# Kernel tuning notes

Hardware: AMD Instinct MI355X
Metric: run time of the kernel (lower is better)

The kernel has to match this reference:

```python
import jax, jax.numpy as jnp
import numpy as np

DIM = 768
N_HEADS = 12
HEAD_DIM = DIM // N_HEADS
B, S = 2, 4096


def setup_inputs() -> dict:
    key = jax.random.key(0)
    k_x, k_wqkv, k_bqkv, k_wout, k_bout = jax.random.split(key, 5)
    scale_in = 1.0 / np.sqrt(DIM)
    return {
        "x": jax.random.normal(k_x, (B, S, DIM), dtype=jnp.float32),
        "Wqkv": jax.random.normal(k_wqkv, (DIM, 3 * DIM), dtype=jnp.float32) * scale_in,
        "bqkv": jax.random.normal(k_bqkv, (3 * DIM,), dtype=jnp.float32) * 0.02,
        "Wout": jax.random.normal(k_wout, (DIM, DIM), dtype=jnp.float32) * scale_in,
        "bout": jax.random.normal(k_bout, (DIM,), dtype=jnp.float32) * 0.02,
    }


def reference(x, Wqkv, bqkv, Wout, bout):
    b, s, d = x.shape
    qkv = (x @ Wqkv + bqkv).reshape(b, s, 3, N_HEADS, HEAD_DIM)
    qkv = jnp.transpose(qkv, (2, 0, 3, 1, 4))  # [3, B, H, S, hd]
    q, k, v = qkv[0], qkv[1], qkv[2]
    scale = HEAD_DIM ** -0.5
    attn = jnp.einsum('bhqd,bhkd->bhqk', q, k) * scale  # [B, H, S, S]
    causal_mask = jnp.triu(jnp.ones((s, s), dtype=bool), k=1)
    attn = jnp.where(causal_mask[None, None], -jnp.inf, attn)
    attn = jax.nn.softmax(attn, axis=-1)
    out = jnp.einsum('bhqk,bhkd->bhqd', attn, v)  # [B, H, S, hd]
    out = jnp.transpose(out, (0, 2, 1, 3)).reshape(b, s, d)
    return out @ Wout + bout
```

## Files before the change

### kernel.cpp

```cpp
#include <hip/hip_runtime.h>
#include <hip/hip_bf16.h>
#include <math.h>

#define DIM 768
#define NH 12
#define HD 64
#define BATCH 2
#define SEQ 4096
#define MTOT (BATCH * SEQ)

#define QSCALE 0.1803368801111244f

typedef unsigned short u16;
typedef __bf16 bf16x8 __attribute__((ext_vector_type(8)));
typedef float  f32x4  __attribute__((ext_vector_type(4)));
typedef float  f32x16 __attribute__((ext_vector_type(16)));
typedef unsigned short u16x4 __attribute__((ext_vector_type(4)));
typedef unsigned short u16x8 __attribute__((ext_vector_type(8)));
typedef unsigned u32x4 __attribute__((ext_vector_type(4)));

__device__ inline u16 f2bf(float f) {
    unsigned u = __builtin_bit_cast(unsigned, f);
    u += 0x7fffu + ((u >> 16) & 1u);
    return (u16)(u >> 16);
}

#if defined(__has_builtin) && __has_builtin(__builtin_amdgcn_cvt_pk_bf16_f32)
#define HAVE_PK_BF16 1
__device__ inline unsigned pk2bf(float a, float b) {
    auto v = __builtin_amdgcn_cvt_pk_bf16_f32(a, b);
    return __builtin_bit_cast(unsigned, v);
}
#else
#define HAVE_PK_BF16 0
__device__ inline unsigned pk2bf(float a, float b) {
    return (unsigned)f2bf(a) | ((unsigned)f2bf(b) << 16);
}
#endif

__device__ inline f32x16 mfma32(bf16x8 a, bf16x8 b, f32x16 c) {
    return __builtin_amdgcn_mfma_f32_32x32x16_bf16(a, b, c, 0, 0, 0);
}

__device__ inline void gl2lds16(const u16* g, u16* l) {
    __builtin_amdgcn_global_load_lds(
        (const __attribute__((address_space(1))) void*)g,
        (__attribute__((address_space(3))) void*)l,
        16, 0, 0);
}

__global__ __launch_bounds__(256)
void prep_fused(const float* __restrict__ x, u16* __restrict__ Xb,
                const float* __restrict__ Wqkv, u16* __restrict__ Wqt,
                const float* __restrict__ Wout, u16* __restrict__ Wot)
{
    const int bid = blockIdx.x;
    if (bid < 3072) {
        const int i = bid * 256 + threadIdx.x;
        float4 a = ((const float4*)x)[i * 2];
        float4 b = ((const float4*)x)[i * 2 + 1];
        u16x8 o;
        o[0] = f2bf(a.x); o[1] = f2bf(a.y); o[2] = f2bf(a.z); o[3] = f2bf(a.w);
        o[4] = f2bf(b.x); o[5] = f2bf(b.y); o[6] = f2bf(b.z); o[7] = f2bf(b.w);
        ((u16x8*)Xb)[i] = o;
        return;
    }
    __shared__ float tile[32][33];
    const float* src; u16* dst; int R, C, bx, by;
    if (bid < 3072 + 1728) {
        const int t2 = bid - 3072;
        src = Wqkv; dst = Wqt; R = 768; C = 2304;
        bx = t2 % 72; by = t2 / 72;
    } else {
        const int t2 = bid - 4800;
        src = Wout; dst = Wot; R = 768; C = 768;
        bx = t2 % 24; by = t2 / 24;
    }
    const int c0 = bx * 32, r0 = by * 32;
    const int tx = threadIdx.x & 31, ty = threadIdx.x >> 5;
#pragma unroll
    for (int i = 0; i < 4; ++i) {
        int row = ty * 4 + i;
        tile[row][tx] = src[(size_t)(r0 + row) * C + c0 + tx];
    }
    __syncthreads();
#pragma unroll
    for (int i = 0; i < 4; ++i) {
        int crow = ty * 4 + i;
        dst[(size_t)(c0 + crow) * R + r0 + tx] = f2bf(tile[tx][crow]);
    }
}

__device__ inline void gemm_lds_mainloop(const u16* __restrict__ Ag,
                                         const u16* __restrict__ Bg,
                                         int m0, int n0, int w, int lane,
                                         u16 (*As)[64 * 64], u16 (*Bs)[64 * 64],
                                         f32x16 acc[2][2])
{
    const int lc32 = lane & 31, hi = lane >> 5;
    const int wm = (w & 1) * 64, wn = (w >> 1) * 64;
    const int drow = lane >> 3;
    const int dp   = lane & 7;

#pragma unroll
    for (int mi = 0; mi < 2; ++mi)
#pragma unroll
        for (int nj = 0; nj < 2; ++nj)
            acc[mi][nj] = f32x16{};

    int trA[2], kcA[2], lr0[2];
#pragma unroll
    for (int i = 0; i < 2; ++i) {
        const int r = w * 16 + i * 8 + drow;
        const int g = dp ^ (r & 7);
        trA[i] = 2 * r + (g >> 2);
        kcA[i] = g & 3;
        lr0[i] = (w * 16 + i * 8) * 64;
    }

#pragma unroll
    for (int i = 0; i < 2; ++i) {
        gl2lds16(Ag + (size_t)(m0 + trA[i]) * 768 + kcA[i] * 8, &As[0][lr0[i]]);
        gl2lds16(Bg + (size_t)(n0 + trA[i]) * 768 + kcA[i] * 8, &Bs[0][lr0[i]]);
    }
#pragma unroll
    for (int i = 0; i < 2; ++i) {
        gl2lds16(Ag + (size_t)(m0 + trA[i]) * 768 + 32 + kcA[i] * 8, &As[1][lr0[i]]);
        gl2lds16(Bg + (size_t)(n0 + trA[i]) * 768 + 32 + kcA[i] * 8, &Bs[1][lr0[i]]);
    }

    int cur = 0;
    for (int ks = 0; ks < 24; ++ks) {
        if (ks + 1 < 24) { asm volatile("s_waitcnt vmcnt(4)" ::: "memory"); }
        else             { asm volatile("s_waitcnt vmcnt(0)" ::: "memory"); }
        __builtin_amdgcn_s_barrier();

        if (ks + 2 < 24) {
            const int nb = (cur >= 1) ? (cur - 1) : 2;
            const int k0 = (ks + 2) * 32;
#pragma unroll
            for (int i = 0; i < 2; ++i) {
                gl2lds16(Ag + (size_t)(m0 + trA[i]) * 768 + k0 + kcA[i] * 8,
                         &As[nb][lr0[i]]);
                gl2lds16(Bg + (size_t)(n0 + trA[i]) * 768 + k0 + kcA[i] * 8,
                         &Bs[nb][lr0[i]]);
            }
        }

        bf16x8 af[2][2], bfr[2][2];
#pragma unroll
        for (int mi = 0; mi < 2; ++mi)
#pragma unroll
            for (int kh = 0; kh < 2; ++kh) {
                const int m = wm + mi * 32 + lc32;
                const int r = m >> 1;
                const int p = ((m & 1) * 4 + kh * 2 + hi) ^ (r & 7);
                af[mi][kh] = *(const bf16x8*)&As[cur][r * 64 + p * 8];
            }
#pragma unroll
        for (int nj = 0; nj < 2; ++nj)
#pragma unroll
            for (int kh = 0; kh < 2; ++kh) {
                const int n = wn + nj * 32 + lc32;
                const int r = n >> 1;
                const int p = ((n & 1) * 4 + kh * 2 + hi) ^ (r & 7);
                bfr[nj][kh] = *(const bf16x8*)&Bs[cur][r * 64 + p * 8];
            }

        __builtin_amdgcn_s_setprio(1);
#pragma unroll
        for (int mi = 0; mi < 2; ++mi)
#pragma unroll
            for (int nj = 0; nj < 2; ++nj) {
                acc[mi][nj] = mfma32(af[mi][0], bfr[nj][0], acc[mi][nj]);
                acc[mi][nj] = mfma32(af[mi][1], bfr[nj][1], acc[mi][nj]);
            }
        __builtin_amdgcn_s_setprio(0);

        cur = (cur == 2) ? 0 : cur + 1;
    }
}

__global__ __launch_bounds__(256, 3)
void gemm_qkv_mfma(const u16* __restrict__ A, const u16* __restrict__ Bt,
                   const float* __restrict__ bias,
                   u16* __restrict__ Qb, u16* __restrict__ Kb, u16* __restrict__ Vt)
{
    __shared__ u16 As[3][64 * 64];
    __shared__ u16 Bs[3][64 * 64];
    const int bid = blockIdx.x;
    const int swz = (bid & 7) * 144 + (bid >> 3);
    const int m0 = (swz / 18) * 128;
    const int n0 = (swz % 18) * 128;
    const int t = threadIdx.x;
    const int w = t >> 6, lane = t & 63;
    const int lc32 = lane & 31, hi = lane >> 5;
    const int wm = (w & 1) * 64, wn = (w >> 1) * 64;

    f32x16 acc[2][2];
    gemm_lds_mainloop(A, Bt, m0, n0, w, lane, As, Bs, acc);

    __syncthreads();

    const int b  = m0 >> 12;
    const int s0 = (m0 & 4095) + wm;
    const int nbase = n0 + wn;
    const int three = nbase / 768;
    const int rem   = nbase - three * 768;
    const int h     = rem >> 6;
    const int bh    = b * NH + h;

    if (three < 2) {
        u16* dst = (three == 0) ? Qb : Kb;
        const float qs = (three == 0) ? QSCALE : 1.0f;
#pragma unroll
        for (int nj = 0; nj < 2; ++nj) {
            const int d = nj * 32 + lc32;
            const float bi = bias[nbase + d];
#pragma unroll
            for (int mi = 0; mi < 2; ++mi)
#pragma unroll
                for (int r = 0; r < 16; ++r) {
                    const int s = s0 + mi * 32 + (r & 3) + 8 * (r >> 2) + 4 * hi;
                    dst[((size_t)bh * SEQ + s) * HD + d] = f2bf((acc[mi][nj][r] + bi) * qs);
                }
        }
    } else {
        u16* scr = (w < 2) ? (&As[0][0] + w * 4352)
                           : (&Bs[0][0] + (w - 2) * 4352);
#pragma unroll
        for (int nj = 0; nj < 2; ++nj) {
            const int d = nj * 32 + lc32;
            const float bi = bias[nbase + d];
#pragma unroll
            for (int mi = 0; mi < 2; ++mi)
#pragma unroll
                for (int r = 0; r < 16; ++r) {
                    const int s = mi * 32 + (r & 3) + 8 * (r >> 2) + 4 * hi;
                    scr[d * 68 + s] = f2bf(acc[mi][nj][r] + bi);
                }
        }
        const size_t vbase = (size_t)bh * HD * SEQ + s0;
#pragma unroll
        for (int p = 0; p < 16; ++p) {
            const int d = p * 4 + (lane >> 4);
            const int s = (lane & 15) * 4;
            u16x4 v4 = *(const u16x4*)&scr[d * 68 + s];
            *(u16x4*)&Vt[vbase + (size_t)d * SEQ + s] = v4;
        }
    }
}

__global__ __launch_bounds__(256, 3)
void gemm_out_mfma(const u16* __restrict__ A, const u16* __restrict__ Bt,
                   const float* __restrict__ bias, float* __restrict__ C)
{
    __shared__ u16 As[3][64 * 64];
    __shared__ u16 Bs[3][32 * 64];
    const int bid = blockIdx.x;
    const int swz = (bid & 7) * 96 + (bid >> 3);
    const int m0 = (swz / 12) * 128;
    const int n0 = (swz % 12) * 64;
    const int t = threadIdx.x;
    const int w = t >> 6, lane = t & 63;
    const int lc32 = lane & 31, hi = lane >> 5;
    const int wm = (w & 1) * 64, wn = (w >> 1) * 32;
    const int drow = lane >> 3;
    const int dp   = lane & 7;

    f32x16 acc[2];
    acc[0] = f32x16{};
    acc[1] = f32x16{};

    int trA[2], kcA[2], lr0[2];
#pragma unroll
    for (int i = 0; i < 2; ++i) {
        const int r = w * 16 + i * 8 + drow;
        const int g = dp ^ (r & 7);
        trA[i] = 2 * r + (g >> 2);
        kcA[i] = g & 3;
        lr0[i] = (w * 16 + i * 8) * 64;
    }
    const int gB  = dp ^ drow;
    const int trB = 2 * (w * 8 + drow) + (gB >> 2);
    const int kcB = gB & 3;
    const int lrB = (w * 8) * 64;

#pragma unroll
    for (int i = 0; i < 2; ++i)
        gl2lds16(A + (size_t)(m0 + trA[i]) * 768 + kcA[i] * 8, &As[0][lr0[i]]);
    gl2lds16(Bt + (size_t)(n0 + trB) * 768 + kcB * 8, &Bs[0][lrB]);
#pragma unroll
    for (int i = 0; i < 2; ++i)
        gl2lds16(A + (size_t)(m0 + trA[i]) * 768 + 32 + kcA[i] * 8, &As[1][lr0[i]]);
    gl2lds16(Bt + (size_t)(n0 + trB) * 768 + 32 + kcB * 8, &Bs[1][lrB]);

    int cur = 0;
    for (int ks = 0; ks < 24; ++ks) {
        if (ks + 1 < 24) { asm volatile("s_waitcnt vmcnt(3)" ::: "memory"); }
        else             { asm volatile("s_waitcnt vmcnt(0)" ::: "memory"); }
        __builtin_amdgcn_s_barrier();

        if (ks + 2 < 24) {
            const int nb = (cur >= 1) ? (cur - 1) : 2;
            const int k0 = (ks + 2) * 32;
#pragma unroll
            for (int i = 0; i < 2; ++i)
                gl2lds16(A + (size_t)(m0 + trA[i]) * 768 + k0 + kcA[i] * 8,
                         &As[nb][lr0[i]]);
            gl2lds16(Bt + (size_t)(n0 + trB) * 768 + k0 + kcB * 8, &Bs[nb][lrB]);
        }

        bf16x8 af[2][2], bfr[2];
#pragma unroll
        for (int mi = 0; mi < 2; ++mi)
#pragma unroll
            for (int kh = 0; kh < 2; ++kh) {
                const int m = wm + mi * 32 + lc32;
                const int r = m >> 1;
                const int p = ((m & 1) * 4 + kh * 2 + hi) ^ (r & 7);
                af[mi][kh] = *(const bf16x8*)&As[cur][r * 64 + p * 8];
            }
#pragma unroll
        for (int kh = 0; kh < 2; ++kh) {
            const int n = wn + lc32;
            const int r = n >> 1;
            const int p = ((n & 1) * 4 + kh * 2 + hi) ^ (r & 7);
            bfr[kh] = *(const bf16x8*)&Bs[cur][r * 64 + p * 8];
        }

        __builtin_amdgcn_s_setprio(1);
#pragma unroll
        for (int mi = 0; mi < 2; ++mi) {
            acc[mi] = mfma32(af[mi][0], bfr[0], acc[mi]);
            acc[mi] = mfma32(af[mi][1], bfr[1], acc[mi]);
        }
        __builtin_amdgcn_s_setprio(0);

        cur = (cur == 2) ? 0 : cur + 1;
    }

    const int col = n0 + wn + lc32;
    const float bi = bias[col];
#pragma unroll
    for (int mi = 0; mi < 2; ++mi)
#pragma unroll
        for (int r = 0; r < 16; ++r) {
            const int row = m0 + wm + mi * 32 + (r & 3) + 8 * (r >> 2) + 4 * hi;
            C[(size_t)row * 768 + col] = acc[mi][r] + bi;
        }
}

__global__ __launch_bounds__(256, 4)
void flash_attn(const u16* __restrict__ Qg, const u16* __restrict__ Kg,
                const u16* __restrict__ Vtg, u16* __restrict__ Og)
{
    const int bh   = blockIdx.x;
    const int qt   = 63 - (int)blockIdx.y;
    const int b    = bh / NH, h = bh % NH;
    const int t    = threadIdx.x;
    const int w    = t >> 6;
    const int wq   = w >> 1;
    const int wk   = w & 1;
    const int lane = t & 63;
    const int lc32 = lane & 31;
    const int hi   = lane >> 5;
    const int drow = lane >> 3;
    const int dp   = lane & 7;

    __shared__ u16 Ks[2][64 * 64];
    __shared__ u16 Vs[2][64 * 64];

    const u16* Qp = Qg  + (size_t)bh * SEQ * HD;
    const u16* Kp = Kg  + (size_t)bh * SEQ * HD;
    const u16* Vp = Vtg + (size_t)bh * HD * SEQ;
    float* Vscr = (float*)&Vs[0][0];
    float* Lx   = (float*)&Ks[0][0];

    const int qrow0 = qt * 64 + wq * 32;

    bf16x8 qa[4];
#pragma unroll
    for (int ds = 0; ds < 4; ++ds)
        qa[ds] = *(const bf16x8*)
            &Qp[(size_t)(qrow0 + lc32) * HD + ds * 16 + hi * 8];

    f32x16 o2[2];
    o2[0] = f32x16{};
    o2[1] = f32x16{};
    float l_r = 0.f;

#pragma unroll
    for (int i = 0; i < 2; ++i) {
        const int r0  = w * 16 + i * 8;
        const int row = r0 + drow;
        const int gc  = dp ^ (row & 7);
        gl2lds16(Kp + (size_t)row * HD + gc * 8, &Ks[0][r0 * 64]);
        gl2lds16(Vp + (size_t)row * SEQ + gc * 8, &Vs[0][r0 * 64]);
    }
    __syncthreads();

    for (int tk = 0; tk <= qt; ++tk) {
        const int kb  = tk * 64;
        const int cur = tk & 1;

        if (tk < qt) {
            const int kbn = kb + 64;
#pragma unroll
            for (int i = 0; i < 2; ++i) {
                const int r0  = w * 16 + i * 8;
                const int row = r0 + drow;
                const int gc  = dp ^ (row & 7);
                gl2lds16(Kp + (size_t)(kbn + row) * HD + gc * 8,
                         &Ks[1 - cur][r0 * 64]);
                gl2lds16(Vp + (size_t)row * SEQ + kbn + gc * 8,
                         &Vs[1 - cur][r0 * 64]);
            }
        }

        f32x16 sacc = {};
        {
            const int row = wk * 32 + lc32;
            const int sw  = row & 7;
            __builtin_amdgcn_s_setprio(1);
#pragma unroll
            for (int ds = 0; ds < 4; ++ds) {
                bf16x8 kf = *(const bf16x8*)
                    &Ks[cur][row * 64 + (((ds * 2 + hi) ^ sw) * 8)];
                sacc = mfma32(kf, qa[ds], sacc);
            }
            __builtin_amdgcn_s_setprio(0);
        }

        if (tk == qt) {
            const int q = qrow0 + lc32;
#pragma unroll
            for (int r = 0; r < 16; ++r) {
                const int key = kb + wk * 32 + (r & 3) + 8 * (r >> 2) + 4 * hi;
                if (key > q) sacc[r] = -1e30f;
            }
        }

        float pv[16];
#pragma unroll
        for (int r = 0; r < 16; ++r)
            pv[r] = __builtin_amdgcn_exp2f(sacc[r]);

        l_r += (((pv[0] + pv[1]) + (pv[2] + pv[3]))
              + ((pv[4] + pv[5]) + (pv[6] + pv[7])))
             + (((pv[8] + pv[9]) + (pv[10] + pv[11]))
              + ((pv[12] + pv[13]) + (pv[14] + pv[15])));

        bf16x8 pa[2];
#pragma unroll
        for (int s = 0; s < 2; ++s) {
            unsigned w0 = pk2bf(pv[8 * s + 0], pv[8 * s + 1]);
            unsigned w1 = pk2bf(pv[8 * s + 2], pv[8 * s + 3]);
            unsigned w2 = pk2bf(pv[8 * s + 4], pv[8 * s + 5]);
            unsigned w3 = pk2bf(pv[8 * s + 6], pv[8 * s + 7]);
            asm("v_permlane32_swap_b32 %0, %1" : "+v"(w0), "+v"(w2));
            asm("v_permlane32_swap_b32 %0, %1" : "+v"(w1), "+v"(w3));
            u32x4 tw;
            tw[0] = w0; tw[1] = w1; tw[2] = w2; tw[3] = w3;
            pa[s] = __builtin_bit_cast(bf16x8, tw);
        }

        __builtin_amdgcn_s_setprio(1);
#pragma unroll
        for (int dt = 0; dt < 2; ++dt) {
            const int row = dt * 32 + lc32;
            const int sw  = row & 7;
#pragma unroll
            for (int s = 0; s < 2; ++s) {
                bf16x8 vf = *(const bf16x8*)
                    &Vs[cur][row * 64 + (((wk * 4 + s * 2 + hi) ^ sw) * 8)];
                o2[dt] = mfma32(pa[s], vf, o2[dt]);
            }
        }
        __builtin_amdgcn_s_setprio(0);

        __syncthreads();
    }

    const float lt = l_r + __shfl_xor(l_r, 32);

    if (wk == 1) {
#pragma unroll
        for (int dt = 0; dt < 2; ++dt)
#pragma unroll
            for (int r = 0; r < 16; ++r) {
                const int ql = (r & 3) + 8 * (r >> 2) + 4 * hi;
                Vscr[wq * 2048 + ql * 64 + dt * 32 + lc32] = o2[dt][r];
            }
        if (lane < 32) Lx[wq * 32 + lc32] = lt;
    }
    __syncthreads();
    if (wk == 0) {
        const float linv_q = 1.0f / (lt + Lx[wq * 32 + lc32]);
#pragma unroll
        for (int r = 0; r < 16; ++r) {
            const int ql   = (r & 3) + 8 * (r >> 2) + 4 * hi;
            const float li = __shfl(linv_q, ql);
            const int q = qrow0 + ql;
            const size_t base = ((size_t)(b * SEQ + q)) * DIM + h * HD + lc32;
#pragma unroll
            for (int dt = 0; dt < 2; ++dt) {
                const float ov = o2[dt][r]
                    + Vscr[wq * 2048 + ql * 64 + dt * 32 + lc32];
                Og[base + dt * 32] = f2bf(ov * li);
            }
        }
    }
}

extern "C" void kernel_launch(void* const* d_in, const int* in_sizes, int n_in,
                              void* d_out, int out_size, void* d_ws, size_t ws_size,
                              hipStream_t stream)
{
    const float* x    = (const float*)d_in[0];
    const float* Wqkv = (const float*)d_in[1];
    const float* bqkv = (const float*)d_in[2];
    const float* Wout = (const float*)d_in[3];
    const float* bout = (const float*)d_in[4];
    float* out = (float*)d_out;

    const size_t NX  = (size_t)MTOT * DIM;
    const size_t NWQ = (size_t)DIM * 3 * DIM;
    const size_t NWO = (size_t)DIM * DIM;
    u16* p   = (u16*)d_ws;
    u16* Xb  = p;              p += NX;
    u16* Wqt = p;              p += NWQ;
    u16* Wot = p;              p += NWO;
    u16* Qb  = p;              p += NX;
    u16* Kb  = p;              p += NX;
    u16* Vt  = p;              p += NX;
    u16* Ao  = p;

    prep_fused<<<3072 + 1728 + 576, 256, 0, stream>>>(x, Xb, Wqkv, Wqt, Wout, Wot);

    gemm_qkv_mfma<<<1152, 256, 0, stream>>>(Xb, Wqt, bqkv, Qb, Kb, Vt);
    flash_attn<<<dim3(24, 64), 256, 0, stream>>>(Qb, Kb, Vt, Ao);
    gemm_out_mfma<<<768, 256, 0, stream>>>(Ao, Wot, bout, out);
}
```

Baseline: 236.1 us.

## Enlarge attention query tile to 128 rows, one 32-row strip per wave

The flash attention block now covers 128 query rows, and each of its four waves processes all 64 keys of every tile for its own 32 query rows. Previously two waves split the keys and merged partial outputs through shared memory at the end. The change doubles K/V tile reuse per load, halves the grid, and removes the cross-wave reduction and its barrier. In exchange each wave holds more registers (occupancy hint lowered to 3), causal waste on the diagonal grows, and there are fewer blocks to balance the triangular work.

Result: no change. 237.8 us (+0.7%).

```diff
diff --git a/kernel.cpp b/kernel.cpp
--- a/kernel.cpp
+++ b/kernel.cpp
@@ -351,17 +351,16 @@
         }
 }
 
-__global__ __launch_bounds__(256, 4)
+__global__ __launch_bounds__(256, 3)
 void flash_attn(const u16* __restrict__ Qg, const u16* __restrict__ Kg,
                 const u16* __restrict__ Vtg, u16* __restrict__ Og)
 {
     const int bh   = blockIdx.x;
-    const int qt   = 63 - (int)blockIdx.y;
+    const int qt   = 31 - (int)blockIdx.y;
+    const int nt   = 2 * qt + 2;
     const int b    = bh / NH, h = bh % NH;
     const int t    = threadIdx.x;
     const int w    = t >> 6;
-    const int wq   = w >> 1;
-    const int wk   = w & 1;
     const int lane = t & 63;
     const int lc32 = lane & 31;
     const int hi   = lane >> 5;
@@ -374,10 +373,8 @@
     const u16* Qp = Qg  + (size_t)bh * SEQ * HD;
     const u16* Kp = Kg  + (size_t)bh * SEQ * HD;
     const u16* Vp = Vtg + (size_t)bh * HD * SEQ;
-    float* Vscr = (float*)&Vs[0][0];
-    float* Lx   = (float*)&Ks[0][0];
-
-    const int qrow0 = qt * 64 + wq * 32;
+
+    const int qrow0 = qt * 128 + w * 32;
 
     bf16x8 qa[4];
 #pragma unroll
@@ -400,11 +397,11 @@
     }
     __syncthreads();
 
-    for (int tk = 0; tk <= qt; ++tk) {
+    for (int tk = 0; tk < nt; ++tk) {
         const int kb  = tk * 64;
         const int cur = tk & 1;
 
-        if (tk < qt) {
+        if (tk + 1 < nt) {
             const int kbn = kb + 64;
 #pragma unroll
             for (int i = 0; i < 2; ++i) {
@@ -418,51 +415,90 @@
             }
         }
 
-        f32x16 sacc = {};
+        f32x16 s0 = {}, s1 = {};
+        __builtin_amdgcn_s_setprio(1);
         {
-            const int row = wk * 32 + lc32;
+            const int row = lc32;
             const int sw  = row & 7;
-            __builtin_amdgcn_s_setprio(1);
 #pragma unroll
             for (int ds = 0; ds < 4; ++ds) {
                 bf16x8 kf = *(const bf16x8*)
                     &Ks[cur][row * 64 + (((ds * 2 + hi) ^ sw) * 8)];
-                sacc = mfma32(kf, qa[ds], sacc);
-            }
-            __builtin_amdgcn_s_setprio(0);
-        }
-
-        if (tk == qt) {
+                s0 = mfma32(kf, qa[ds], s0);
+            }
+        }
+        {
+            const int row = 32 + lc32;
+            const int sw  = row & 7;
+#pragma unroll
+            for (int ds = 0; ds < 4; ++ds) {
+                bf16x8 kf = *(const bf16x8*)
+                    &Ks[cur][row * 64 + (((ds * 2 + hi) ^ sw) * 8)];
+                s1 = mfma32(kf, qa[ds], s1);
+            }
+        }
+        __builtin_amdgcn_s_setprio(0);
+
+        {
             const int q = qrow0 + lc32;
-#pragma unroll
-            for (int r = 0; r < 16; ++r) {
-                const int key = kb + wk * 32 + (r & 3) + 8 * (r >> 2) + 4 * hi;
-                if (key > q) sacc[r] = -1e30f;
-            }
-        }
-
-        float pv[16];
-#pragma unroll
-        for (int r = 0; r < 16; ++r)
-            pv[r] = __builtin_amdgcn_exp2f(sacc[r]);
-
-        l_r += (((pv[0] + pv[1]) + (pv[2] + pv[3]))
-              + ((pv[4] + pv[5]) + (pv[6] + pv[7])))
-             + (((pv[8] + pv[9]) + (pv[10] + pv[11]))
-              + ((pv[12] + pv[13]) + (pv[14] + pv[15])));
-
-        bf16x8 pa[2];
-#pragma unroll
-        for (int s = 0; s < 2; ++s) {
-            unsigned w0 = pk2bf(pv[8 * s + 0], pv[8 * s + 1]);
-            unsigned w1 = pk2bf(pv[8 * s + 2], pv[8 * s + 3]);
-            unsigned w2 = pk2bf(pv[8 * s + 4], pv[8 * s + 5]);
-            unsigned w3 = pk2bf(pv[8 * s + 6], pv[8 * s + 7]);
-            asm("v_permlane32_swap_b32 %0, %1" : "+v"(w0), "+v"(w2));
-            asm("v_permlane32_swap_b32 %0, %1" : "+v"(w1), "+v"(w3));
-            u32x4 tw;
-            tw[0] = w0; tw[1] = w1; tw[2] = w2; tw[3] = w3;
-            pa[s] = __builtin_bit_cast(bf16x8, tw);
+            if (kb + 31 > qrow0) {
+#pragma unroll
+                for (int r = 0; r < 16; ++r) {
+                    const int key = kb + (r & 3) + 8 * (r >> 2) + 4 * hi;
+                    if (key > q) s0[r] = -1e30f;
+                }
+            }
+            if (kb + 63 > qrow0) {
+#pragma unroll
+                for (int r = 0; r < 16; ++r) {
+                    const int key = kb + 32 + (r & 3) + 8 * (r >> 2) + 4 * hi;
+                    if (key > q) s1[r] = -1e30f;
+                }
+            }
+        }
+
+        bf16x8 pa[4];
+        {
+            float pv[16];
+#pragma unroll
+            for (int r = 0; r < 16; ++r) pv[r] = __builtin_amdgcn_exp2f(s0[r]);
+            l_r += (((pv[0] + pv[1]) + (pv[2] + pv[3]))
+                  + ((pv[4] + pv[5]) + (pv[6] + pv[7])))
+                 + (((pv[8] + pv[9]) + (pv[10] + pv[11]))
+                  + ((pv[12] + pv[13]) + (pv[14] + pv[15])));
+#pragma unroll
+            for (int s = 0; s < 2; ++s) {
+                unsigned w0 = pk2bf(pv[8 * s + 0], pv[8 * s + 1]);
+                unsigned w1 = pk2bf(pv[8 * s + 2], pv[8 * s + 3]);
+                unsigned w2 = pk2bf(pv[8 * s + 4], pv[8 * s + 5]);
+                unsigned w3 = pk2bf(pv[8 * s + 6], pv[8 * s + 7]);
+                asm("v_permlane32_swap_b32 %0, %1" : "+v"(w0), "+v"(w2));
+                asm("v_permlane32_swap_b32 %0, %1" : "+v"(w1), "+v"(w3));
+                u32x4 tw;
+                tw[0] = w0; tw[1] = w1; tw[2] = w2; tw[3] = w3;
+                pa[s] = __builtin_bit_cast(bf16x8, tw);
+            }
+        }
+        {
+            float pv[16];
+#pragma unroll
+            for (int r = 0; r < 16; ++r) pv[r] = __builtin_amdgcn_exp2f(s1[r]);
+            l_r += (((pv[0] + pv[1]) + (pv[2] + pv[3]))
+                  + ((pv[4] + pv[5]) + (pv[6] + pv[7])))
+                 + (((pv[8] + pv[9]) + (pv[10] + pv[11]))
+                  + ((pv[12] + pv[13]) + (pv[14] + pv[15])));
+#pragma unroll
+            for (int s = 0; s < 2; ++s) {
+                unsigned w0 = pk2bf(pv[8 * s + 0], pv[8 * s + 1]);
+                unsigned w1 = pk2bf(pv[8 * s + 2], pv[8 * s + 3]);
+                unsigned w2 = pk2bf(pv[8 * s + 4], pv[8 * s + 5]);
+                unsigned w3 = pk2bf(pv[8 * s + 6], pv[8 * s + 7]);
+                asm("v_permlane32_swap_b32 %0, %1" : "+v"(w0), "+v"(w2));
+                asm("v_permlane32_swap_b32 %0, %1" : "+v"(w1), "+v"(w3));
+                u32x4 tw;
+                tw[0] = w0; tw[1] = w1; tw[2] = w2; tw[3] = w3;
+                pa[2 + s] = __builtin_bit_cast(bf16x8, tw);
+            }
         }
 
         __builtin_amdgcn_s_setprio(1);
@@ -471,10 +507,10 @@
             const int row = dt * 32 + lc32;
             const int sw  = row & 7;
 #pragma unroll
-            for (int s = 0; s < 2; ++s) {
+            for (int ks = 0; ks < 4; ++ks) {
                 bf16x8 vf = *(const bf16x8*)
-                    &Vs[cur][row * 64 + (((wk * 4 + s * 2 + hi) ^ sw) * 8)];
-                o2[dt] = mfma32(pa[s], vf, o2[dt]);
+                    &Vs[cur][row * 64 + (((ks * 2 + hi) ^ sw) * 8)];
+                o2[dt] = mfma32(pa[ks], vf, o2[dt]);
             }
         }
         __builtin_amdgcn_s_setprio(0);
@@ -483,33 +519,16 @@
     }
 
     const float lt = l_r + __shfl_xor(l_r, 32);
-
-    if (wk == 1) {
-#pragma unroll
-        for (int dt = 0; dt < 2; ++dt)
-#pragma unroll
-            for (int r = 0; r < 16; ++r) {
-                const int ql = (r & 3) + 8 * (r >> 2) + 4 * hi;
-                Vscr[wq * 2048 + ql * 64 + dt * 32 + lc32] = o2[dt][r];
-            }
-        if (lane < 32) Lx[wq * 32 + lc32] = lt;
-    }
-    __syncthreads();
-    if (wk == 0) {
-        const float linv_q = 1.0f / (lt + Lx[wq * 32 + lc32]);
-#pragma unroll
-        for (int r = 0; r < 16; ++r) {
-            const int ql   = (r & 3) + 8 * (r >> 2) + 4 * hi;
-            const float li = __shfl(linv_q, ql);
-            const int q = qrow0 + ql;
-            const size_t base = ((size_t)(b * SEQ + q)) * DIM + h * HD + lc32;
-#pragma unroll
-            for (int dt = 0; dt < 2; ++dt) {
-                const float ov = o2[dt][r]
-                    + Vscr[wq * 2048 + ql * 64 + dt * 32 + lc32];
-                Og[base + dt * 32] = f2bf(ov * li);
-            }
-        }
+    const float linv_q = 1.0f / lt;
+
+#pragma unroll
+    for (int r = 0; r < 16; ++r) {
+        const int ql   = (r & 3) + 8 * (r >> 2) + 4 * hi;
+        const float li = __shfl(linv_q, ql);
+        const int q = qrow0 + ql;
+        const size_t base = ((size_t)(b * SEQ + q)) * DIM + h * HD + lc32;
+        Og[base]      = f2bf(o2[0][r] * li);
+        Og[base + 32] = f2bf(o2[1][r] * li);
     }
 }
 
@@ -539,6 +558,6 @@
     prep_fused<<<3072 + 1728 + 576, 256, 0, stream>>>(x, Xb, Wqkv, Wqt, Wout, Wot);
 
     gemm_qkv_mfma<<<1152, 256, 0, stream>>>(Xb, Wqt, bqkv, Qb, Kb, Vt);
-    flash_attn<<<dim3(24, 64), 256, 0, stream>>>(Qb, Kb, Vt, Ao);
+    flash_attn<<<dim3(24, 32), 256, 0, stream>>>(Qb, Kb, Vt, Ao);
     gemm_out_mfma<<<768, 256, 0, stream>>>(Ao, Wot, bout, out);
 }
```
